# Performance work log

Hardware: AMD Instinct MI355X
Metric: run time of the kernel (lower is better)

The kernel has to match this reference:

```python
import jax, jax.numpy as jnp
import numpy as np
from jax import lax

LATENT = 128
CODEBOOK = 1024

def _conv(x, w, b):
    # NCHW conv, kernel OIHW, stride 1, padding 1 (same)
    y = lax.conv_general_dilated(x, w, (1, 1), ((1, 1), (1, 1)),
                                 dimension_numbers=('NCHW', 'OIHW', 'NCHW'))
    return y + b[None, :, None, None]

def _conv_transpose(x, w, b):
    # ConvTranspose2d(k=3, s=1, p=1) == conv with flipped kernel, in/out swapped, pad 1
    w_eff = jnp.flip(w, (2, 3)).transpose(1, 0, 2, 3)  # [Cin,Cout,3,3] -> [Cout,Cin,3,3]
    return _conv(x, w_eff, b)

def _maxpool2(x):
    return lax.reduce_window(x, -jnp.inf, lax.max, (1, 1, 2, 2), (1, 1, 2, 2), 'VALID')

def _upsample2(x):
    # F.interpolate(scale_factor=2), default nearest
    return jnp.repeat(jnp.repeat(x, 2, axis=2), 2, axis=3)

def setup_inputs() -> dict:
    key = jax.random.key(0)
    ks = jax.random.split(key, 20)
    f = jnp.float32
    inp = {
        'x': jax.random.uniform(ks[0], (8192, 1, 24, 24), dtype=f),
        'conv1_w': jax.random.normal(ks[1], (32, 1, 3, 3), f) * 0.1,
        'conv1_b': jnp.zeros((32,), f),
        'conv2_w': jax.random.normal(ks[2], (64, 32, 3, 3), f) * 0.05,
        'conv2_b': jnp.zeros((64,), f),
        'conv3_w': jax.random.normal(ks[3], (128, 64, 3, 3), f) * 0.04,
        'conv3_b': jnp.zeros((128,), f),
        'enc_fc_w': jax.random.normal(ks[4], (LATENT, 3 * 3 * 128), f) * 0.03,
        'enc_fc_b': jnp.zeros((LATENT,), f),
        'codebook': jax.random.normal(ks[5], (CODEBOOK, LATENT), f),
        'dec_fc_w': jax.random.normal(ks[6], (3 * 3 * 128, LATENT), f) * 0.09,
        'dec_fc_b': jnp.zeros((3 * 3 * 128,), f),
        'dct1_w': jax.random.normal(ks[7], (128, 64, 3, 3), f) * 0.03,  # [Cin,Cout,kh,kw]
        'dct1_b': jnp.zeros((64,), f),
        'dct2_w': jax.random.normal(ks[8], (64, 32, 3, 3), f) * 0.04,
        'dct2_b': jnp.zeros((32,), f),
        'dct3_w': jax.random.normal(ks[9], (32, 1, 3, 3), f) * 0.06,
        'dct3_b': jnp.zeros((1,), f),
    }
    return inp

def reference(x, conv1_w, conv1_b, conv2_w, conv2_b, conv3_w, conv3_b,
              enc_fc_w, enc_fc_b, codebook, dec_fc_w, dec_fc_b,
              dct1_w, dct1_b, dct2_w, dct2_b, dct3_w, dct3_b):
    # ---- Encoder ----
    h = _maxpool2(jax.nn.relu(_conv(x, conv1_w, conv1_b)))     # [B,32,12,12]
    h = _maxpool2(jax.nn.relu(_conv(h, conv2_w, conv2_b)))     # [B,64,6,6]
    h = _maxpool2(jax.nn.relu(_conv(h, conv3_w, conv3_b)))     # [B,128,3,3]
    z = h.reshape(-1, 3 * 3 * 128) @ enc_fc_w.T + enc_fc_b     # [B,128]
    # ---- Quantize (L2 nearest-codeword; matmul-trick distances, same argmin) ----
    d2 = (jnp.sum(z * z, axis=1, keepdims=True)
          - 2.0 * z @ codebook.T
          + jnp.sum(codebook * codebook, axis=1)[None, :])     # [B,K]
    idx = jnp.argmin(d2, axis=1)                               # [B]
    z_q = codebook[idx]                                        # [B,128]
    # ---- Decoder ----
    d = z_q @ dec_fc_w.T + dec_fc_b                            # [B,1152]
    d = d.reshape(-1, 128, 3, 3)
    d = _upsample2(jax.nn.relu(_conv_transpose(d, dct1_w, dct1_b)))  # [B,64,6,6]
    d = _upsample2(jax.nn.relu(_conv_transpose(d, dct2_w, dct2_b)))  # [B,32,12,12]
    d = _upsample2(jax.nn.relu(_conv_transpose(d, dct3_w, dct3_b)))  # [B,1,24,24]
    return d
```

## Files before the change

### kernel.cpp

```cpp
#include <hip/hip_runtime.h>

typedef __attribute__((ext_vector_type(8))) short short8;
typedef __attribute__((ext_vector_type(4))) float f32x4;
typedef unsigned short ushort_t;
typedef unsigned int uint_t;

#define OFF_W1R   0
#define OFF_W2R   288
#define OFF_W3R   (288+18432)
#define OFF_EWT   (18720+73728)
#define OFF_CT    (92448+147456)
#define OFF_CC    (239904+131072)
#define OFF_DWT   (370976+1024)
#define OFF_D1R   (372000+147456)
#define OFF_D2R   (519456+73728)
#define OFF_D3R   (593184+18432)
#define WS_WEIGHTS (611616+288)
#define OFF_W2BF  WS_WEIGHTS
#define OFF_W3BF  (OFF_W2BF+18432)
#define OFF_H     (OFF_W3BF+73728)
#define OFF_TABLE OFF_H
#define OFF_IDSN  (OFF_H+8192*1152)

__device__ __forceinline__ ushort_t f2bf(float v) {
  uint_t u = __float_as_uint(v);
  return (ushort_t)((u + 0x7FFFu + ((u >> 16) & 1u)) >> 16);
}
__device__ __forceinline__ float bf2f(ushort_t b) {
  return __uint_as_float(((uint_t)b) << 16);
}

__global__ void vq_prep(const float* __restrict__ conv1_w, const float* __restrict__ codebook,
                        const float* __restrict__ dec_fc_w,
                        const float* __restrict__ dct1_w, const float* __restrict__ dct2_w,
                        const float* __restrict__ dct3_w, float* __restrict__ ws) {
  int i = blockIdx.x * blockDim.x + threadIdx.x;
  if (i >= WS_WEIGHTS) return;
  if (i < OFF_W2R) {
    int tap = i >> 5, co = i & 31;
    ws[i] = conv1_w[co*9 + tap];
  } else if (i < OFF_CC) {
    return;
  } else if (i < OFF_DWT) {
    int k = i - OFF_CC;
    float s = 0.f;
    for (int j = 0; j < 128; ++j) { float v = codebook[k*128+j]; s += v*v; }
    ws[i] = s;
  } else if (i < OFF_D1R) {
    int l = i - OFF_DWT;
    int j = l % 1152, k = l / 1152;
    ws[i] = dec_fc_w[j*128 + k];
  } else if (i < OFF_D2R) {
    int l = i - OFF_D1R;
    int co = l & 63, r = l >> 6, tap = r % 9, ci = r / 9;
    ws[i] = dct1_w[(ci*64 + co)*9 + (8 - tap)];
  } else if (i < OFF_D3R) {
    int l = i - OFF_D2R;
    int co = l & 31, r = l >> 5, tap = r % 9, ci = r / 9;
    ws[i] = dct2_w[(ci*32 + co)*9 + (8 - tap)];
  } else {
    int l = i - OFF_D3R;
    int tap = l % 9, ci = l / 9;
    ws[i] = dct3_w[ci*9 + (8 - tap)];
  }
}

#define P2_N (92160 + 294912 + 262144)
__global__ void vq_prep2(const float* __restrict__ conv2_w, const float* __restrict__ conv3_w,
                         const float* __restrict__ enc_fc_w, const float* __restrict__ codebook,
                         float* __restrict__ ws) {
  int i = blockIdx.x * blockDim.x + threadIdx.x;
  if (i >= P2_N) return;
  ushort_t* W2 = (ushort_t*)(ws + OFF_W2BF);
  ushort_t* W3 = (ushort_t*)(ws + OFF_W3BF);
  ushort_t* EW = (ushort_t*)(ws + OFF_EWT);
  ushort_t* CB = (ushort_t*)(ws + OFF_CT);
  if (i < 18432) {
    int tap = i >> 11, r = i & 2047, co = r >> 5, ch = r & 31;
    float v = conv2_w[(co*32 + ch)*9 + tap];
    ushort_t hb = f2bf(v);
    W2[i] = hb; W2[18432 + i] = f2bf(v - bf2f(hb));
  } else if (i < 92160) {
    int j = i - 18432;
    int tap = j >> 13, r = j & 8191, co = r >> 6, ch = r & 63;
    float v = conv3_w[(co*64 + ch)*9 + tap];
    ushort_t hb = f2bf(v);
    W3[j] = hb; W3[73728 + j] = f2bf(v - bf2f(hb));
  } else if (i < 92160 + 294912) {
    int e = i - 92160;
    int p = e / 147456, r = e % 147456;
    int kk = r & 31, n = (r >> 5) & 127, ks = r >> 12;
    float v = enc_fc_w[n*1152 + ks*32 + kk];
    ushort_t hb = f2bf(v);
    EW[r] = (p == 0) ? EW[r] : EW[r];
    if (p == 0) EW[r] = hb; else EW[147456 + r] = f2bf(v - bf2f(hb));
  } else {
    int e = i - 92160 - 294912;
    int p = e / 131072, r = e % 131072;
    int kk = r & 31, cw = (r >> 5) & 1023, ks = r >> 15;
    float v = codebook[cw*128 + ks*32 + kk];
    ushort_t hb = f2bf(v);
    if (p == 0) CB[r] = hb; else CB[131072 + r] = f2bf(v - bf2f(hb));
  }
}

__global__ __launch_bounds__(256, 3) void vq_enc(
    const float* __restrict__ x,
    const float* __restrict__ b1, const float* __restrict__ b2, const float* __restrict__ b3,
    const float* __restrict__ ws, ushort_t* __restrict__ hhi, ushort_t* __restrict__ hlo)
{
  __shared__ ushort_t R0h[7840], R0l[7840];
  __shared__ ushort_t C3h[4608], C3l[4608];
  __shared__ float XT[624];
  const int t = threadIdx.x;
  const int b = blockIdx.x;

  for (int i = t; i < 3920; i += 256) { ((uint_t*)R0h)[i] = 0u; ((uint_t*)R0l)[i] = 0u; }
  for (int i = t; i < 2304; i += 256) { ((uint_t*)C3h)[i] = 0u; ((uint_t*)C3l)[i] = 0u; }
  const float* xb = x + (size_t)b * 576;
  for (int i = t; i < 624; i += 256) {
    int row = i / 26, col = i - row * 26;
    XT[i] = (col >= 1 && col <= 24) ? xb[row*24 + col - 1] : 0.f;
  }
  __syncthreads();

  {
    int co = t & 31, g = t >> 5, gy = g >> 1, gx = g & 1;
    float w[9];
    #pragma unroll
    for (int k = 0; k < 9; ++k) w[k] = ws[OFF_W1R + k*32 + co];
    float bias = b1[co];
    #pragma unroll
    for (int pr = 0; pr < 3; ++pr) {
      int Y = gy*6 + pr*2;
      float a0[12], a1[12];
      #pragma unroll
      for (int i = 0; i < 12; ++i) { a0[i] = 0.f; a1[i] = 0.f; }
      #pragma unroll
      for (int wy = 0; wy < 4; ++wy) {
        int ry = Y - 1 + wy;
        if (ry < 0 || ry > 23) continue;
        const float2* rp = (const float2*)&XT[ry*26 + gx*12];
        float r[14];
        #pragma unroll
        for (int k = 0; k < 7; ++k) { float2 p = rp[k]; r[2*k] = p.x; r[2*k+1] = p.y; }
        if (wy < 3) {
          #pragma unroll
          for (int xx = 0; xx < 12; ++xx)
            #pragma unroll
            for (int dx = 0; dx < 3; ++dx) a0[xx] += r[xx+dx] * w[wy*3+dx];
        }
        if (wy >= 1) {
          #pragma unroll
          for (int xx = 0; xx < 12; ++xx)
            #pragma unroll
            for (int dx = 0; dx < 3; ++dx) a1[xx] += r[xx+dx] * w[(wy-1)*3+dx];
        }
      }
      #pragma unroll
      for (int pc = 0; pc < 6; ++pc) {
        float m = fmaxf(fmaxf(a0[2*pc], a0[2*pc+1]), fmaxf(a1[2*pc], a1[2*pc+1]));
        float v = m + bias; v = v > 0.f ? v : 0.f;
        int row = gy*3 + pr, colp = gx*6 + pc;
        int addr = ((row+1)*14 + (colp+1))*40 + co;
        ushort_t hb = f2bf(v);
        R0h[addr] = hb;
        R0l[addr] = f2bf(v - bf2f(hb));
      }
    }
  }
  __syncthreads();

  const int lane = t & 63, quad = lane >> 4, col = lane & 15;
  const int wv = t >> 6;

  {
    const int h = wv & 1, p = wv >> 1;
    const ushort_t* W2 = (const ushort_t*)(ws + OFF_W2BF);
    int baseA[5];
    #pragma unroll
    for (int mi = 0; mi < 5; ++mi) {
      int m = (h*5 + mi)*16 + col; if (m > 143) m = 143;
      int cell = m >> 2, sub = m & 3;
      int opy = cell / 6, opx = cell - opy*6;
      int y = 2*opy + (sub >> 1), xx = 2*opx + (sub & 1);
      baseA[mi] = (y*14 + xx)*40 + quad*8;
    }
    f32x4 acc[5][2];
    #pragma unroll
    for (int mi = 0; mi < 5; ++mi) { acc[mi][0] = (f32x4)0.f; acc[mi][1] = (f32x4)0.f; }
    const int co0 = p*32 + col, co1 = co0 + 16;
    #pragma unroll
    for (int t9 = 0; t9 < 9; ++t9) {
      const int TAPOFF = ((t9/3)*14 + (t9%3))*40;
      int bidx = t9*2048 + quad*8;
      short8 Bh0 = *(const short8*)(W2 + bidx + co0*32);
      short8 Bh1 = *(const short8*)(W2 + bidx + co1*32);
      short8 Bl0 = *(const short8*)(W2 + 18432 + bidx + co0*32);
      short8 Bl1 = *(const short8*)(W2 + 18432 + bidx + co1*32);
      #pragma unroll
      for (int mi = 0; mi < 5; ++mi) {
        int a = baseA[mi] + TAPOFF;
        short8 Ah = *(const short8*)(R0h + a);
        short8 Al = *(const short8*)(R0l + a);
        acc[mi][0] = __builtin_amdgcn_mfma_f32_16x16x32_bf16(Al, Bh0, acc[mi][0], 0, 0, 0);
        acc[mi][0] = __builtin_amdgcn_mfma_f32_16x16x32_bf16(Ah, Bl0, acc[mi][0], 0, 0, 0);
        acc[mi][0] = __builtin_amdgcn_mfma_f32_16x16x32_bf16(Ah, Bh0, acc[mi][0], 0, 0, 0);
        acc[mi][1] = __builtin_amdgcn_mfma_f32_16x16x32_bf16(Al, Bh1, acc[mi][1], 0, 0, 0);
        acc[mi][1] = __builtin_amdgcn_mfma_f32_16x16x32_bf16(Ah, Bl1, acc[mi][1], 0, 0, 0);
        acc[mi][1] = __builtin_amdgcn_mfma_f32_16x16x32_bf16(Ah, Bh1, acc[mi][1], 0, 0, 0);
      }
    }
    #pragma unroll
    for (int mi = 0; mi < 5; ++mi) {
      int cell = (h*5 + mi)*4 + quad;
      if (cell < 36) {
        int opy = cell / 6, opx = cell - opy*6;
        int wa = ((opy+1)*8 + (opx+1))*72;
        #pragma unroll
        for (int j = 0; j < 2; ++j) {
          int ch = j ? co1 : co0;
          f32x4 a = acc[mi][j];
          float v = fmaxf(fmaxf(a.x, a.y), fmaxf(a.z, a.w)) + b2[ch];
          v = v > 0.f ? v : 0.f;
          ushort_t hb = f2bf(v);
          C3h[wa + ch] = hb;
          C3l[wa + ch] = f2bf(v - bf2f(hb));
        }
      }
    }
  }
  __syncthreads();

  {
    const ushort_t* W3 = (const ushort_t*)(ws + OFF_W3BF);
    int baseA[3];
    #pragma unroll
    for (int mt = 0; mt < 3; ++mt) {
      int m = mt*16 + col; if (m > 35) m = 35;
      int cell = m >> 2, sub = m & 3;
      int opy = cell / 3, opx = cell - opy*3;
      int y = 2*opy + (sub >> 1), xx = 2*opx + (sub & 1);
      baseA[mt] = (y*8 + xx)*72 + quad*8;
    }
    f32x4 acc[3][2];
    #pragma unroll
    for (int mt = 0; mt < 3; ++mt) { acc[mt][0] = (f32x4)0.f; acc[mt][1] = (f32x4)0.f; }
    const int co0 = wv*16 + col, co1 = co0 + 64;
    #pragma unroll
    for (int ks = 0; ks < 18; ++ks) {
      const int t9 = ks >> 1, ch0 = (ks & 1)*32;
      const int TAPOFF = ((t9/3)*8 + (t9%3))*72;
      int bidx = t9*8192 + ch0 + quad*8;
      short8 Bh0 = *(const short8*)(W3 + bidx + co0*64);
      short8 Bh1 = *(const short8*)(W3 + bidx + co1*64);
      short8 Bl0 = *(const short8*)(W3 + 73728 + bidx + co0*64);
      short8 Bl1 = *(const short8*)(W3 + 73728 + bidx + co1*64);
      #pragma unroll
      for (int mt = 0; mt < 3; ++mt) {
        int a = baseA[mt] + TAPOFF + ch0;
        short8 Ah = *(const short8*)(C3h + a);
        short8 Al = *(const short8*)(C3l + a);
        acc[mt][0] = __builtin_amdgcn_mfma_f32_16x16x32_bf16(Al, Bh0, acc[mt][0], 0, 0, 0);
        acc[mt][0] = __builtin_amdgcn_mfma_f32_16x16x32_bf16(Ah, Bl0, acc[mt][0], 0, 0, 0);
        acc[mt][0] = __builtin_amdgcn_mfma_f32_16x16x32_bf16(Ah, Bh0, acc[mt][0], 0, 0, 0);
        acc[mt][1] = __builtin_amdgcn_mfma_f32_16x16x32_bf16(Al, Bh1, acc[mt][1], 0, 0, 0);
        acc[mt][1] = __builtin_amdgcn_mfma_f32_16x16x32_bf16(Ah, Bl1, acc[mt][1], 0, 0, 0);
        acc[mt][1] = __builtin_amdgcn_mfma_f32_16x16x32_bf16(Ah, Bh1, acc[mt][1], 0, 0, 0);
      }
    }
    ushort_t* hb_ = hhi + (size_t)b * 1152;
    ushort_t* lb_ = hlo + (size_t)b * 1152;
    #pragma unroll
    for (int mt = 0; mt < 3; ++mt) {
      int cell = mt*4 + quad;
      if (cell < 9) {
        #pragma unroll
        for (int j = 0; j < 2; ++j) {
          int ch = j ? co1 : co0;
          f32x4 a = acc[mt][j];
          float v = fmaxf(fmaxf(a.x, a.y), fmaxf(a.z, a.w)) + b3[ch];
          v = v > 0.f ? v : 0.f;
          ushort_t hb2 = f2bf(v);
          hb_[ch*9 + cell] = hb2;
          lb_[ch*9 + cell] = f2bf(v - bf2f(hb2));
        }
      }
    }
  }
}

__global__ __launch_bounds__(256, 4) void vq_fc_argmin(
    const float* __restrict__ efb, const float* __restrict__ ws,
    const ushort_t* __restrict__ hhi, const ushort_t* __restrict__ hlo,
    int* __restrict__ ids)
{
  __shared__ float ZL[16*132];
  __shared__ float WVs[64];
  __shared__ int   WIs[64];
  const int t = threadIdx.x;
  const int sb = blockIdx.x * 16;
  const int lane = t & 63, wv = t >> 6;
  const int col = lane & 15, quad = lane >> 4;

  const ushort_t* EW  = (const ushort_t*)(ws + OFF_EWT);
  const ushort_t* CBB = (const ushort_t*)(ws + OFF_CT);

  f32x4 acc0 = (f32x4)0.f, acc1 = (f32x4)0.f;
  const size_t hrow = (size_t)(sb + col) * 1152 + quad*8;
  #pragma unroll 4
  for (int ks = 0; ks < 36; ++ks) {
    short8 Ah = *(const short8*)(hhi + hrow + ks*32);
    short8 Al = *(const short8*)(hlo + hrow + ks*32);
    int n0 = wv*32 + col, n1 = n0 + 16;
    const ushort_t* bp0 = EW + (ks*128 + n0)*32 + quad*8;
    const ushort_t* bp1 = EW + (ks*128 + n1)*32 + quad*8;
    short8 Bh0 = *(const short8*)(bp0);
    short8 Bl0 = *(const short8*)(bp0 + 147456);
    short8 Bh1 = *(const short8*)(bp1);
    short8 Bl1 = *(const short8*)(bp1 + 147456);
    acc0 = __builtin_amdgcn_mfma_f32_16x16x32_bf16(Al, Bh0, acc0, 0, 0, 0);
    acc0 = __builtin_amdgcn_mfma_f32_16x16x32_bf16(Ah, Bl0, acc0, 0, 0, 0);
    acc0 = __builtin_amdgcn_mfma_f32_16x16x32_bf16(Ah, Bh0, acc0, 0, 0, 0);
    acc1 = __builtin_amdgcn_mfma_f32_16x16x32_bf16(Al, Bh1, acc1, 0, 0, 0);
    acc1 = __builtin_amdgcn_mfma_f32_16x16x32_bf16(Ah, Bl1, acc1, 0, 0, 0);
    acc1 = __builtin_amdgcn_mfma_f32_16x16x32_bf16(Ah, Bh1, acc1, 0, 0, 0);
  }
  {
    int n0 = wv*32 + col, n1 = n0 + 16;
    float bs0 = efb[n0], bs1 = efb[n1];
    #pragma unroll
    for (int r = 0; r < 4; ++r) {
      int m = quad*4 + r;
      ZL[m*132 + n0] = acc0[r] + bs0;
      ZL[m*132 + n1] = acc1[r] + bs1;
    }
  }
  __syncthreads();

  short8 zAh[4], zAl[4];
  #pragma unroll
  for (int ks = 0; ks < 4; ++ks) {
    const float* zp = &ZL[col*132 + ks*32 + quad*8];
    float4 z0 = *(const float4*)zp;
    float4 z1 = *(const float4*)(zp + 4);
    float zv[8] = {z0.x, z0.y, z0.z, z0.w, z1.x, z1.y, z1.z, z1.w};
    ushort_t ph[8], pl[8];
    #pragma unroll
    for (int e = 0; e < 8; ++e) {
      ushort_t hb = f2bf(zv[e]);
      ph[e] = hb; pl[e] = f2bf(zv[e] - bf2f(hb));
    }
    zAh[ks] = *(const short8*)ph;
    zAl[ks] = *(const short8*)pl;
  }

  float bestv[4]; int besti[4];
  #pragma unroll
  for (int r = 0; r < 4; ++r) { bestv[r] = 3.4e38f; besti[r] = 0; }
  for (int c4 = 0; c4 < 4; ++c4) {
    f32x4 dacc[4];
    #pragma unroll
    for (int nn = 0; nn < 4; ++nn) dacc[nn] = (f32x4)0.f;
    #pragma unroll
    for (int ks = 0; ks < 4; ++ks) {
      #pragma unroll
      for (int nn = 0; nn < 4; ++nn) {
        int cw = (wv*16 + c4*4 + nn)*16 + col;
        const ushort_t* bp = CBB + (size_t)(ks*1024 + cw)*32 + quad*8;
        short8 Bh = *(const short8*)bp;
        short8 Bl = *(const short8*)(bp + 131072);
        dacc[nn] = __builtin_amdgcn_mfma_f32_16x16x32_bf16(zAl[ks], Bh, dacc[nn], 0, 0, 0);
        dacc[nn] = __builtin_amdgcn_mfma_f32_16x16x32_bf16(zAh[ks], Bl, dacc[nn], 0, 0, 0);
        dacc[nn] = __builtin_amdgcn_mfma_f32_16x16x32_bf16(zAh[ks], Bh, dacc[nn], 0, 0, 0);
      }
    }
    #pragma unroll
    for (int nn = 0; nn < 4; ++nn) {
      int cw = (wv*16 + c4*4 + nn)*16 + col;
      float ccv = ws[OFF_CC + cw];
      #pragma unroll
      for (int r = 0; r < 4; ++r) {
        float dist = ccv - 2.f*dacc[nn][r];
        if (dist < bestv[r]) { bestv[r] = dist; besti[r] = cw; }
      }
    }
  }

  #pragma unroll
  for (int r = 0; r < 4; ++r) {
    float v = bestv[r]; int ii = besti[r];
    #pragma unroll
    for (int off = 8; off >= 1; off >>= 1) {
      float v2 = __shfl_xor(v, off); int i2 = __shfl_xor(ii, off);
      if (v2 < v || (v2 == v && i2 < ii)) { v = v2; ii = i2; }
    }
    if (col == 0) {
      int m = quad*4 + r;
      WVs[wv*16 + m] = v; WIs[wv*16 + m] = ii;
    }
  }
  __syncthreads();
  if (t < 16) {
    float v = WVs[t]; int ii = WIs[t];
    #pragma unroll
    for (int w2 = 1; w2 < 4; ++w2) {
      float v2 = WVs[w2*16 + t]; int i2 = WIs[w2*16 + t];
      if (v2 < v || (v2 == v && i2 < ii)) { v = v2; ii = i2; }
    }
    ids[sb + t] = ii;
  }
}

__global__ __launch_bounds__(256, 4) void vq_dec_table(
    const float* __restrict__ codebook, const float* __restrict__ decb,
    const float* __restrict__ d1b, const float* __restrict__ d2b, const float* __restrict__ d3b,
    const float* __restrict__ ws, float* __restrict__ table)
{
  __shared__ float DB[1152];
  __shared__ float R1[2432];
  __shared__ float R0[4736];
  __shared__ float ZQ[128];
  const int t = threadIdx.x;
  const int cw = blockIdx.x;

  if (t < 128) ZQ[t] = codebook[(size_t)cw*128 + t];
  __syncthreads();

  #pragma unroll
  for (int p = 0; p < 5; ++p) {
    int j = t + p*256;
    if (j < 1152) {
      float a0 = decb[j];
      const float* wb = ws + OFF_DWT + j;
      #pragma unroll 4
      for (int k = 0; k < 128; ++k) a0 += wb[k*1152] * ZQ[k];
      DB[j] = a0;
    }
  }
  __syncthreads();

  {
    int co = t & 63, g = t >> 6;
    float a9[9];
    #pragma unroll
    for (int i = 0; i < 9; ++i) a9[i] = 0.f;
    const float* wbase = ws + OFF_D1R + co;
    for (int ci = g*32; ci < g*32+32; ++ci) {
      float w[9];
      #pragma unroll
      for (int k = 0; k < 9; ++k) w[k] = wbase[(ci*9+k)*64];
      const float* fin = DB + ci*9;
      #pragma unroll
      for (int ry = 0; ry < 3; ++ry) {
        float r[5];
        r[0] = 0.f; r[4] = 0.f;
        r[1] = fin[ry*3]; r[2] = fin[ry*3+1]; r[3] = fin[ry*3+2];
        #pragma unroll
        for (int y = 0; y < 3; ++y) {
          int d = ry - y + 1;
          if (d >= 0 && d < 3) {
            #pragma unroll
            for (int xx = 0; xx < 3; ++xx)
              #pragma unroll
              for (int dx = 0; dx < 3; ++dx) a9[y*3+xx] += r[xx+dx] * w[d*3+dx];
          }
        }
      }
    }
    __syncthreads();
    if (g) {
      #pragma unroll
      for (int i = 0; i < 9; ++i) R0[((g-1)*64 + co)*9 + i] = a9[i];
    }
    __syncthreads();
    if (!g) {
      float bias = d1b[co];
      #pragma unroll
      for (int i = 0; i < 9; ++i)
        a9[i] += R0[co*9 + i] + R0[(64+co)*9 + i] + R0[(128+co)*9 + i];
      #pragma unroll
      for (int yy = 0; yy < 3; ++yy)
        #pragma unroll
        for (int xx = 0; xx < 3; ++xx) {
          float v = a9[yy*3+xx] + bias; v = v > 0.f ? v : 0.f;
          int base = co*38 + (2*yy)*6 + 2*xx;
          R1[base] = v; R1[base+1] = v; R1[base+6] = v; R1[base+7] = v;
        }
    }
  }
  __syncthreads();

  {
    int co = t & 31, hh = (t >> 5) & 1, g = t >> 6;
    int sy = g >> 1, sx = g & 1;
    float a9[9];
    #pragma unroll
    for (int i = 0; i < 9; ++i) a9[i] = 0.f;
    const float* wbase = ws + OFF_D2R + co;
    for (int ci = hh*32; ci < hh*32+32; ++ci) {
      float w[9];
      #pragma unroll
      for (int k = 0; k < 9; ++k) w[k] = wbase[(ci*9+k)*32];
      const float* base = &R1[ci*38];
      #pragma unroll
      for (int wy = 0; wy < 5; ++wy) {
        int ry = sy*3 - 1 + wy;
        if (ry < 0 || ry > 5) continue;
        const float* row = base + ry*6 + sx*3;
        float r[5];
        if (sx == 0) {
          r[0] = 0.f; r[1] = row[0]; r[2] = row[1]; r[3] = row[2]; r[4] = row[3];
        } else {
          r[0] = row[-1]; r[1] = row[0]; r[2] = row[1]; r[3] = row[2]; r[4] = 0.f;
        }
        #pragma unroll
        for (int y = 0; y < 3; ++y) {
          int d = wy - 1 - y + 1;
          if (d >= 0 && d < 3) {
            #pragma unroll
            for (int xx = 0; xx < 3; ++xx)
              #pragma unroll
              for (int dx = 0; dx < 3; ++dx) a9[y*3+xx] += r[xx+dx] * w[d*3+dx];
          }
        }
      }
    }
    __syncthreads();
    if (hh) {
      #pragma unroll
      for (int i = 0; i < 9; ++i) DB[(g*32 + co)*9 + i] = a9[i];
    }
    __syncthreads();
    if (!hh) {
      float bias = d2b[co];
      #pragma unroll
      for (int i = 0; i < 9; ++i) a9[i] += DB[(g*32 + co)*9 + i];
      #pragma unroll
      for (int yy = 0; yy < 3; ++yy)
        #pragma unroll
        for (int xx = 0; xx < 3; ++xx) {
          float v = a9[yy*3+xx] + bias; v = v > 0.f ? v : 0.f;
          int rr = sy*3 + yy, cc_ = sx*3 + xx;
          int base = co*146 + (2*rr)*12 + 2*cc_;
          R0[base] = v; R0[base+1] = v; R0[base+12] = v; R0[base+13] = v;
        }
    }
  }
  __syncthreads();

  if (t < 144) {
    int yy = t / 12, xx = t - yy*12;
    const float* w3 = ws + OFF_D3R;
    float acc = d3b[0];
    for (int ci = 0; ci < 32; ++ci) {
      const float* base = &R0[ci*146];
      #pragma unroll
      for (int dy = 0; dy < 3; ++dy) {
        int ry = yy - 1 + dy;
        int ryc = ry < 0 ? 0 : (ry > 11 ? 11 : ry);
        bool rok = (ry >= 0 && ry < 12);
        #pragma unroll
        for (int dx = 0; dx < 3; ++dx) {
          int rx = xx - 1 + dx;
          int rxc = rx < 0 ? 0 : (rx > 11 ? 11 : rx);
          float v = base[ryc*12 + rxc];
          v = (rok && rx >= 0 && rx < 12) ? v : 0.f;
          acc += v * w3[ci*9 + dy*3 + dx];
        }
      }
    }
    float v = acc > 0.f ? acc : 0.f;
    float* ob = table + (size_t)cw * 576;
    int o0 = (2*yy)*24 + 2*xx;
    ob[o0] = v; ob[o0+1] = v; ob[o0+24] = v; ob[o0+25] = v;
  }
}

__global__ __launch_bounds__(256, 8) void vq_scatter(
    const float* __restrict__ table, const int* __restrict__ ids,
    float* __restrict__ out, int nvec)
{
  int idx = blockIdx.x * 256 + threadIdx.x;
  if (idx >= nvec) return;
  int b = idx / 144;
  int r = idx - b * 144;
  int cw = ids[b];
  ((float4*)out)[idx] = ((const float4*)(table + (size_t)cw * 576))[r];
}

extern "C" void kernel_launch(void* const* d_in, const int* in_sizes, int n_in,
                              void* d_out, int out_size, void* d_ws, size_t ws_size,
                              hipStream_t stream) {
  const float* x   = (const float*)d_in[0];
  const float* c1w = (const float*)d_in[1];
  const float* c1b = (const float*)d_in[2];
  const float* c2w = (const float*)d_in[3];
  const float* c2b = (const float*)d_in[4];
  const float* c3w = (const float*)d_in[5];
  const float* c3b = (const float*)d_in[6];
  const float* efw = (const float*)d_in[7];
  const float* efb = (const float*)d_in[8];
  const float* cb  = (const float*)d_in[9];
  const float* dfw = (const float*)d_in[10];
  const float* dfb = (const float*)d_in[11];
  const float* dw1 = (const float*)d_in[12];
  const float* db1 = (const float*)d_in[13];
  const float* dw2 = (const float*)d_in[14];
  const float* db2 = (const float*)d_in[15];
  const float* dw3 = (const float*)d_in[16];
  const float* db3 = (const float*)d_in[17];
  float* ws = (float*)d_ws;
  ushort_t* hhi  = (ushort_t*)(ws + OFF_H);
  ushort_t* hlo  = hhi + (size_t)8192*1152;
  float* table = ws + OFF_TABLE;
  int*   ids   = (int*)(ws + OFF_IDSN);
  float* outp = (float*)d_out;
  int B = in_sizes[0] / 576;

  vq_prep<<<(WS_WEIGHTS + 255) / 256, 256, 0, stream>>>(c1w, cb, dfw, dw1, dw2, dw3, ws);
  vq_prep2<<<(P2_N + 255) / 256, 256, 0, stream>>>(c2w, c3w, efw, cb, ws);
  vq_enc<<<B, 256, 0, stream>>>(x, c1b, c2b, c3b, ws, hhi, hlo);
  vq_fc_argmin<<<B/16, 256, 0, stream>>>(efb, ws, hhi, hlo, ids);
  vq_dec_table<<<1024, 256, 0, stream>>>(cb, dfb, db1, db2, db3, ws, table);
  int nvec = B * 144;
  vq_scatter<<<(nvec + 255) / 256, 256, 0, stream>>>(table, ids, outp, nvec);
}
```

Measured before the change: 634.1 us.

## Move decoder table convs to split-bf16 MFMA and re-layout encoder LDS tiles

The per-codeword decoder table kernel now runs the first two transposed convolutions as implicit GEMMs on MFMA, using three bf16 hi/lo products per step, with weights pre-split by the prep kernel. The scalar FP32 loops are dropped and the last conv reads an upsampled, padded channel-last buffer. The encoder's shared-memory activations are reorganised into channel-group-major tiles that hold 8 channels per pixel, and conv1 writes packed channel pairs, which shrinks LDS use and may cut bank conflicts. The split-bf16 scheme gives slightly different rounding than FP32.

```diff
diff --git a/kernel.cpp b/kernel.cpp
--- a/kernel.cpp
+++ b/kernel.cpp
@@ -6,8 +6,8 @@
 typedef unsigned int uint_t;
 
 #define OFF_W1R   0
-#define OFF_W2R   288
-#define OFF_W3R   (288+18432)
+#define OFF_BD2F  288
+#define OFF_BD1F  18720
 #define OFF_EWT   (18720+73728)
 #define OFF_CT    (92448+147456)
 #define OFF_CC    (239904+131072)
@@ -31,12 +31,11 @@
 }
 
 __global__ void vq_prep(const float* __restrict__ conv1_w, const float* __restrict__ codebook,
-                        const float* __restrict__ dec_fc_w,
-                        const float* __restrict__ dct1_w, const float* __restrict__ dct2_w,
-                        const float* __restrict__ dct3_w, float* __restrict__ ws) {
+                        const float* __restrict__ dec_fc_w, const float* __restrict__ dct3_w,
+                        float* __restrict__ ws) {
   int i = blockIdx.x * blockDim.x + threadIdx.x;
   if (i >= WS_WEIGHTS) return;
-  if (i < OFF_W2R) {
+  if (i < OFF_BD2F) {
     int tap = i >> 5, co = i & 31;
     ws[i] = conv1_w[co*9 + tap];
   } else if (i < OFF_CC) {
@@ -50,31 +49,28 @@
     int l = i - OFF_DWT;
     int j = l % 1152, k = l / 1152;
     ws[i] = dec_fc_w[j*128 + k];
-  } else if (i < OFF_D2R) {
-    int l = i - OFF_D1R;
-    int co = l & 63, r = l >> 6, tap = r % 9, ci = r / 9;
-    ws[i] = dct1_w[(ci*64 + co)*9 + (8 - tap)];
   } else if (i < OFF_D3R) {
-    int l = i - OFF_D2R;
-    int co = l & 31, r = l >> 5, tap = r % 9, ci = r / 9;
-    ws[i] = dct2_w[(ci*32 + co)*9 + (8 - tap)];
-  } else {
+    return;
+  } else if (i < WS_WEIGHTS) {
     int l = i - OFF_D3R;
     int tap = l % 9, ci = l / 9;
     ws[i] = dct3_w[ci*9 + (8 - tap)];
   }
 }
 
-#define P2_N (92160 + 294912 + 262144)
+#define P2_N (92160 + 294912 + 262144 + 73728 + 18432)
 __global__ void vq_prep2(const float* __restrict__ conv2_w, const float* __restrict__ conv3_w,
                          const float* __restrict__ enc_fc_w, const float* __restrict__ codebook,
+                         const float* __restrict__ dct1_w, const float* __restrict__ dct2_w,
                          float* __restrict__ ws) {
   int i = blockIdx.x * blockDim.x + threadIdx.x;
   if (i >= P2_N) return;
-  ushort_t* W2 = (ushort_t*)(ws + OFF_W2BF);
-  ushort_t* W3 = (ushort_t*)(ws + OFF_W3BF);
-  ushort_t* EW = (ushort_t*)(ws + OFF_EWT);
-  ushort_t* CB = (ushort_t*)(ws + OFF_CT);
+  ushort_t* W2  = (ushort_t*)(ws + OFF_W2BF);
+  ushort_t* W3  = (ushort_t*)(ws + OFF_W3BF);
+  ushort_t* EW  = (ushort_t*)(ws + OFF_EWT);
+  ushort_t* CB  = (ushort_t*)(ws + OFF_CT);
+  ushort_t* BD1 = (ushort_t*)(ws + OFF_BD1F);
+  ushort_t* BD2 = (ushort_t*)(ws + OFF_BD2F);
   if (i < 18432) {
     int tap = i >> 11, r = i & 2047, co = r >> 5, ch = r & 31;
     float v = conv2_w[(co*32 + ch)*9 + tap];
@@ -86,21 +82,34 @@
     float v = conv3_w[(co*64 + ch)*9 + tap];
     ushort_t hb = f2bf(v);
     W3[j] = hb; W3[73728 + j] = f2bf(v - bf2f(hb));
-  } else if (i < 92160 + 294912) {
-    int e = i - 92160;
-    int p = e / 147456, r = e % 147456;
+  } else if (i < 387072) {
+    int r = i - 92160;
+    int p = r / 147456; r %= 147456;
     int kk = r & 31, n = (r >> 5) & 127, ks = r >> 12;
     float v = enc_fc_w[n*1152 + ks*32 + kk];
     ushort_t hb = f2bf(v);
-    EW[r] = (p == 0) ? EW[r] : EW[r];
     if (p == 0) EW[r] = hb; else EW[147456 + r] = f2bf(v - bf2f(hb));
-  } else {
-    int e = i - 92160 - 294912;
-    int p = e / 131072, r = e % 131072;
+  } else if (i < 649216) {
+    int r = i - 387072;
+    int p = r / 131072; r %= 131072;
     int kk = r & 31, cw = (r >> 5) & 1023, ks = r >> 15;
     float v = codebook[cw*128 + ks*32 + kk];
     ushort_t hb = f2bf(v);
     if (p == 0) CB[r] = hb; else CB[131072 + r] = f2bf(v - bf2f(hb));
+  } else if (i < 722944) {
+    int r = i - 649216;
+    int co = r / 1152, k = r - co*1152;
+    int tap = k >> 7, ci = k & 127;
+    float v = dct1_w[(ci*64 + co)*9 + (8 - tap)];
+    ushort_t hb = f2bf(v);
+    BD1[r] = hb; BD1[73728 + r] = f2bf(v - bf2f(hb));
+  } else {
+    int r = i - 722944;
+    int co = r / 576, k = r - co*576;
+    int tap = k >> 6, ci = k & 63;
+    float v = dct2_w[(ci*32 + co)*9 + (8 - tap)];
+    ushort_t hb = f2bf(v);
+    BD2[r] = hb; BD2[18432 + r] = f2bf(v - bf2f(hb));
   }
 }
 
@@ -109,63 +118,81 @@
     const float* __restrict__ b1, const float* __restrict__ b2, const float* __restrict__ b3,
     const float* __restrict__ ws, ushort_t* __restrict__ hhi, ushort_t* __restrict__ hlo)
 {
-  __shared__ ushort_t R0h[7840], R0l[7840];
-  __shared__ ushort_t C3h[4608], C3l[4608];
+  __shared__ ushort_t R0h[6272], R0l[6272];
+  __shared__ ushort_t A2h[5120], A2l[5120];
   __shared__ float XT[624];
   const int t = threadIdx.x;
   const int b = blockIdx.x;
 
-  for (int i = t; i < 3920; i += 256) { ((uint_t*)R0h)[i] = 0u; ((uint_t*)R0l)[i] = 0u; }
-  for (int i = t; i < 2304; i += 256) { ((uint_t*)C3h)[i] = 0u; ((uint_t*)C3l)[i] = 0u; }
+  for (int i = t; i < 3136; i += 256) { ((uint_t*)R0h)[i] = 0u; ((uint_t*)R0l)[i] = 0u; }
+  for (int i = t; i < 2560; i += 256) { ((uint_t*)A2h)[i] = 0u; ((uint_t*)A2l)[i] = 0u; }
   const float* xb = x + (size_t)b * 576;
   for (int i = t; i < 624; i += 256) {
-    int row = i / 26, col = i - row * 26;
-    XT[i] = (col >= 1 && col <= 24) ? xb[row*24 + col - 1] : 0.f;
+    int row = i / 26, c = i - row * 26;
+    XT[i] = (c >= 1 && c <= 24) ? xb[row*24 + c - 1] : 0.f;
   }
   __syncthreads();
 
   {
-    int co = t & 31, g = t >> 5, gy = g >> 1, gx = g & 1;
-    float w[9];
-    #pragma unroll
-    for (int k = 0; k < 9; ++k) w[k] = ws[OFF_W1R + k*32 + co];
-    float bias = b1[co];
+    int cp = t & 15, g = t >> 4;
+    int gy = g >> 2, gx = g & 3;
+    float wgt[2][9], bs[2];
+    #pragma unroll
+    for (int c = 0; c < 2; ++c) {
+      bs[c] = b1[2*cp + c];
+      #pragma unroll
+      for (int k = 0; k < 9; ++k) wgt[c][k] = ws[OFF_W1R + k*32 + 2*cp + c];
+    }
+    int quadc = cp >> 2, coff = (cp & 3) * 2;
     #pragma unroll
     for (int pr = 0; pr < 3; ++pr) {
-      int Y = gy*6 + pr*2;
-      float a0[12], a1[12];
-      #pragma unroll
-      for (int i = 0; i < 12; ++i) { a0[i] = 0.f; a1[i] = 0.f; }
+      int Y = (gy*3 + pr)*2;
+      float a0[2][6], a1[2][6];
+      #pragma unroll
+      for (int c = 0; c < 2; ++c)
+        #pragma unroll
+        for (int i = 0; i < 6; ++i) { a0[c][i] = 0.f; a1[c][i] = 0.f; }
       #pragma unroll
       for (int wy = 0; wy < 4; ++wy) {
         int ry = Y - 1 + wy;
         if (ry < 0 || ry > 23) continue;
-        const float2* rp = (const float2*)&XT[ry*26 + gx*12];
-        float r[14];
+        const float2* rp = (const float2*)&XT[ry*26 + gx*6];
+        float r[8];
         #pragma unroll
-        for (int k = 0; k < 7; ++k) { float2 p = rp[k]; r[2*k] = p.x; r[2*k+1] = p.y; }
+        for (int k = 0; k < 4; ++k) { float2 p = rp[k]; r[2*k] = p.x; r[2*k+1] = p.y; }
         if (wy < 3) {
           #pragma unroll
-          for (int xx = 0; xx < 12; ++xx)
+          for (int c = 0; c < 2; ++c)
             #pragma unroll
-            for (int dx = 0; dx < 3; ++dx) a0[xx] += r[xx+dx] * w[wy*3+dx];
+            for (int xx = 0; xx < 6; ++xx)
+              #pragma unroll
+              for (int dx = 0; dx < 3; ++dx) a0[c][xx] += r[xx+dx] * wgt[c][wy*3+dx];
         }
         if (wy >= 1) {
           #pragma unroll
-          for (int xx = 0; xx < 12; ++xx)
+          for (int c = 0; c < 2; ++c)
             #pragma unroll
-            for (int dx = 0; dx < 3; ++dx) a1[xx] += r[xx+dx] * w[(wy-1)*3+dx];
+            for (int xx = 0; xx < 6; ++xx)
+              #pragma unroll
+              for (int dx = 0; dx < 3; ++dx) a1[c][xx] += r[xx+dx] * wgt[c][(wy-1)*3+dx];
         }
       }
       #pragma unroll
-      for (int pc = 0; pc < 6; ++pc) {
-        float m = fmaxf(fmaxf(a0[2*pc], a0[2*pc+1]), fmaxf(a1[2*pc], a1[2*pc+1]));
-        float v = m + bias; v = v > 0.f ? v : 0.f;
-        int row = gy*3 + pr, colp = gx*6 + pc;
-        int addr = ((row+1)*14 + (colp+1))*40 + co;
-        ushort_t hb = f2bf(v);
-        R0h[addr] = hb;
-        R0l[addr] = f2bf(v - bf2f(hb));
+      for (int pc = 0; pc < 3; ++pc) {
+        uint_t hi = 0, lo = 0;
+        #pragma unroll
+        for (int c = 0; c < 2; ++c) {
+          float m = fmaxf(fmaxf(a0[c][2*pc], a0[c][2*pc+1]), fmaxf(a1[c][2*pc], a1[c][2*pc+1]));
+          float v = m + bs[c]; v = v > 0.f ? v : 0.f;
+          ushort_t hb = f2bf(v);
+          ushort_t lb = f2bf(v - bf2f(hb));
+          hi |= ((uint_t)hb) << (16*c);
+          lo |= ((uint_t)lb) << (16*c);
+        }
+        int p = (gy*3 + pr + 1)*14 + (gx*3 + pc + 1);
+        int base = quadc*1568 + p*8 + coff;
+        ((uint_t*)R0h)[base >> 1] = hi;
+        ((uint_t*)R0l)[base >> 1] = lo;
       }
     }
   }
@@ -177,14 +204,14 @@
   {
     const int h = wv & 1, p = wv >> 1;
     const ushort_t* W2 = (const ushort_t*)(ws + OFF_W2BF);
-    int baseA[5];
+    int pA[5];
     #pragma unroll
     for (int mi = 0; mi < 5; ++mi) {
       int m = (h*5 + mi)*16 + col; if (m > 143) m = 143;
       int cell = m >> 2, sub = m & 3;
       int opy = cell / 6, opx = cell - opy*6;
       int y = 2*opy + (sub >> 1), xx = 2*opx + (sub & 1);
-      baseA[mi] = (y*14 + xx)*40 + quad*8;
+      pA[mi] = y*14 + xx;
     }
     f32x4 acc[5][2];
     #pragma unroll
@@ -192,7 +219,7 @@
     const int co0 = p*32 + col, co1 = co0 + 16;
     #pragma unroll
     for (int t9 = 0; t9 < 9; ++t9) {
-      const int TAPOFF = ((t9/3)*14 + (t9%3))*40;
+      const int toff = (t9/3)*14 + (t9%3);
       int bidx = t9*2048 + quad*8;
       short8 Bh0 = *(const short8*)(W2 + bidx + co0*32);
       short8 Bh1 = *(const short8*)(W2 + bidx + co1*32);
@@ -200,7 +227,7 @@
       short8 Bl1 = *(const short8*)(W2 + 18432 + bidx + co1*32);
       #pragma unroll
       for (int mi = 0; mi < 5; ++mi) {
-        int a = baseA[mi] + TAPOFF;
+        int a = quad*1568 + (pA[mi] + toff)*8;
         short8 Ah = *(const short8*)(R0h + a);
         short8 Al = *(const short8*)(R0l + a);
         acc[mi][0] = __builtin_amdgcn_mfma_f32_16x16x32_bf16(Al, Bh0, acc[mi][0], 0, 0, 0);
@@ -216,7 +243,7 @@
       int cell = (h*5 + mi)*4 + quad;
       if (cell < 36) {
         int opy = cell / 6, opx = cell - opy*6;
-        int wa = ((opy+1)*8 + (opx+1))*72;
+        int p2 = (opy+1)*10 + (opx+1);
         #pragma unroll
         for (int j = 0; j < 2; ++j) {
           int ch = j ? co1 : co0;
@@ -224,8 +251,9 @@
           float v = fmaxf(fmaxf(a.x, a.y), fmaxf(a.z, a.w)) + b2[ch];
           v = v > 0.f ? v : 0.f;
           ushort_t hb = f2bf(v);
-          C3h[wa + ch] = hb;
-          C3l[wa + ch] = f2bf(v - bf2f(hb));
+          int wa = (ch >> 3)*640 + p2*8 + (ch & 7);
+          A2h[wa] = hb;
+          A2l[wa] = f2bf(v - bf2f(hb));
         }
       }
     }
@@ -234,14 +262,14 @@
 
   {
     const ushort_t* W3 = (const ushort_t*)(ws + OFF_W3BF);
-    int baseA[3];
+    int pA[3];
     #pragma unroll
     for (int mt = 0; mt < 3; ++mt) {
       int m = mt*16 + col; if (m > 35) m = 35;
       int cell = m >> 2, sub = m & 3;
       int opy = cell / 3, opx = cell - opy*3;
       int y = 2*opy + (sub >> 1), xx = 2*opx + (sub & 1);
-      baseA[mt] = (y*8 + xx)*72 + quad*8;
+      pA[mt] = y*10 + xx;
     }
     f32x4 acc[3][2];
     #pragma unroll
@@ -249,8 +277,9 @@
     const int co0 = wv*16 + col, co1 = co0 + 64;
     #pragma unroll
     for (int ks = 0; ks < 18; ++ks) {
-      const int t9 = ks >> 1, ch0 = (ks & 1)*32;
-      const int TAPOFF = ((t9/3)*8 + (t9%3))*72;
+      const int t9 = ks >> 1, half = ks & 1, ch0 = half*32;
+      const int toff = (t9/3)*10 + (t9%3);
+      const int grp = half*4 + quad;
       int bidx = t9*8192 + ch0 + quad*8;
       short8 Bh0 = *(const short8*)(W3 + bidx + co0*64);
       short8 Bh1 = *(const short8*)(W3 + bidx + co1*64);
@@ -258,9 +287,9 @@
       short8 Bl1 = *(const short8*)(W3 + 73728 + bidx + co1*64);
       #pragma unroll
       for (int mt = 0; mt < 3; ++mt) {
-        int a = baseA[mt] + TAPOFF + ch0;
-        short8 Ah = *(const short8*)(C3h + a);
-        short8 Al = *(const short8*)(C3l + a);
+        int a = grp*640 + (pA[mt] + toff)*8;
+        short8 Ah = *(const short8*)(A2h + a);
+        short8 Al = *(const short8*)(A2l + a);
         acc[mt][0] = __builtin_amdgcn_mfma_f32_16x16x32_bf16(Al, Bh0, acc[mt][0], 0, 0, 0);
         acc[mt][0] = __builtin_amdgcn_mfma_f32_16x16x32_bf16(Ah, Bl0, acc[mt][0], 0, 0, 0);
         acc[mt][0] = __builtin_amdgcn_mfma_f32_16x16x32_bf16(Ah, Bh0, acc[mt][0], 0, 0, 0);
@@ -417,13 +446,21 @@
     const float* __restrict__ d1b, const float* __restrict__ d2b, const float* __restrict__ d3b,
     const float* __restrict__ ws, float* __restrict__ table)
 {
-  __shared__ float DB[1152];
-  __shared__ float R1[2432];
-  __shared__ float R0[4736];
+  __shared__ float POOL[8008];
+  __shared__ float PS[1536];
   __shared__ float ZQ[128];
+  ushort_t* FAh = (ushort_t*)POOL;
+  ushort_t* FAl = FAh + 3400;
+  ushort_t* GAh = (ushort_t*)(POOL + 3400);
+  ushort_t* GAl = GAh + 4608;
+  float* R2 = POOL;
+
   const int t = threadIdx.x;
   const int cw = blockIdx.x;
-
+  const int lane = t & 63, wv = t >> 6;
+  const int col = lane & 15, quad = lane >> 4;
+
+  for (int i = t; i < 8008; i += 256) POOL[i] = 0.f;
   if (t < 128) ZQ[t] = codebook[(size_t)cw*128 + t];
   __syncthreads();
 
@@ -435,116 +472,112 @@
       const float* wb = ws + OFF_DWT + j;
       #pragma unroll 4
       for (int k = 0; k < 128; ++k) a0 += wb[k*1152] * ZQ[k];
-      DB[j] = a0;
-    }
-  }
-  __syncthreads();
-
+      int ci = j / 9, rem = j - ci*9;
+      int pix = ((rem/3)+1)*5 + (rem%3) + 1;
+      ushort_t hb = f2bf(a0);
+      FAh[pix*136 + ci] = hb;
+      FAl[pix*136 + ci] = f2bf(a0 - bf2f(hb));
+    }
+  }
+  __syncthreads();
+
+  const ushort_t* BD1 = (const ushort_t*)(ws + OFF_BD1F);
+  f32x4 acc1 = (f32x4)0.f;
   {
-    int co = t & 63, g = t >> 6;
-    float a9[9];
-    #pragma unroll
-    for (int i = 0; i < 9; ++i) a9[i] = 0.f;
-    const float* wbase = ws + OFF_D1R + co;
-    for (int ci = g*32; ci < g*32+32; ++ci) {
-      float w[9];
-      #pragma unroll
-      for (int k = 0; k < 9; ++k) w[k] = wbase[(ci*9+k)*64];
-      const float* fin = DB + ci*9;
-      #pragma unroll
-      for (int ry = 0; ry < 3; ++ry) {
-        float r[5];
-        r[0] = 0.f; r[4] = 0.f;
-        r[1] = fin[ry*3]; r[2] = fin[ry*3+1]; r[3] = fin[ry*3+2];
-        #pragma unroll
-        for (int y = 0; y < 3; ++y) {
-          int d = ry - y + 1;
-          if (d >= 0 && d < 3) {
-            #pragma unroll
-            for (int xx = 0; xx < 3; ++xx)
-              #pragma unroll
-              for (int dx = 0; dx < 3; ++dx) a9[y*3+xx] += r[xx+dx] * w[d*3+dx];
-          }
+    const int m9 = col < 9 ? col : 8;
+    const int oy = m9/3, ox = m9 - oy*3;
+    const int co = wv*16 + col;
+    #pragma unroll 4
+    for (int ks = 0; ks < 36; ++ks) {
+      int kb = ks*32 + quad*8;
+      int tap = kb >> 7, ci0 = kb & 127;
+      int pix = (oy + tap/3)*5 + ox + tap%3;
+      short8 Ah = *(const short8*)(FAh + pix*136 + ci0);
+      short8 Al = *(const short8*)(FAl + pix*136 + ci0);
+      const ushort_t* bp = BD1 + co*1152 + kb;
+      short8 Bh = *(const short8*)bp;
+      short8 Bl = *(const short8*)(bp + 73728);
+      acc1 = __builtin_amdgcn_mfma_f32_16x16x32_bf16(Al, Bh, acc1, 0, 0, 0);
+      acc1 = __builtin_amdgcn_mfma_f32_16x16x32_bf16(Ah, Bl, acc1, 0, 0, 0);
+      acc1 = __builtin_amdgcn_mfma_f32_16x16x32_bf16(Ah, Bh, acc1, 0, 0, 0);
+    }
+  }
+  {
+    const int co = wv*16 + col;
+    float bias = d1b[co];
+    #pragma unroll
+    for (int r = 0; r < 4; ++r) {
+      int m = quad*4 + r;
+      if (m < 9) {
+        int oy = m/3, ox = m - oy*3;
+        float v = acc1[r] + bias; v = v > 0.f ? v : 0.f;
+        ushort_t hb = f2bf(v), lb = f2bf(v - bf2f(hb));
+        int rbase = (2*oy+1)*8 + (2*ox+1);
+        GAh[(rbase  )*72 + co] = hb; GAh[(rbase+1)*72 + co] = hb;
+        GAh[(rbase+8)*72 + co] = hb; GAh[(rbase+9)*72 + co] = hb;
+        GAl[(rbase  )*72 + co] = lb; GAl[(rbase+1)*72 + co] = lb;
+        GAl[(rbase+8)*72 + co] = lb; GAl[(rbase+9)*72 + co] = lb;
+      }
+    }
+  }
+  __syncthreads();
+
+  const ushort_t* BD2 = (const ushort_t*)(ws + OFF_BD2F);
+  f32x4 acc2[3];
+  acc2[0] = (f32x4)0.f; acc2[1] = (f32x4)0.f; acc2[2] = (f32x4)0.f;
+  const int h = wv >> 1, js = (wv & 1)*3;
+  for (int ks = h*9; ks < h*9 + 9; ++ks) {
+    int kb = ks*32 + quad*8;
+    int tap = kb >> 6, ci0 = kb & 63;
+    int ty = tap/3, tx = tap - ty*3;
+    #pragma unroll
+    for (int jj = 0; jj < 3; ++jj) {
+      int job = js + jj;
+      int mt = job >> 1, nt = job & 1;
+      int m = mt*16 + col; if (m > 35) m = 35;
+      int oy = m/6, ox = m - oy*6;
+      int pix = (oy+ty)*8 + ox+tx;
+      short8 Ah = *(const short8*)(GAh + pix*72 + ci0);
+      short8 Al = *(const short8*)(GAl + pix*72 + ci0);
+      int co = nt*16 + col;
+      const ushort_t* bp = BD2 + co*576 + kb;
+      short8 Bh = *(const short8*)bp;
+      short8 Bl = *(const short8*)(bp + 18432);
+      acc2[jj] = __builtin_amdgcn_mfma_f32_16x16x32_bf16(Al, Bh, acc2[jj], 0, 0, 0);
+      acc2[jj] = __builtin_amdgcn_mfma_f32_16x16x32_bf16(Ah, Bl, acc2[jj], 0, 0, 0);
+      acc2[jj] = __builtin_amdgcn_mfma_f32_16x16x32_bf16(Ah, Bh, acc2[jj], 0, 0, 0);
+    }
+  }
+  __syncthreads();
+  if (h == 1) {
+    #pragma unroll
+    for (int jj = 0; jj < 3; ++jj) {
+      int job = js + jj;
+      #pragma unroll
+      for (int r = 0; r < 4; ++r) PS[(job*64 + lane)*4 + r] = acc2[jj][r];
+    }
+  }
+  for (int i = t; i < 6468; i += 256) R2[i] = 0.f;
+  __syncthreads();
+  if (h == 0) {
+    #pragma unroll
+    for (int jj = 0; jj < 3; ++jj) {
+      int job = js + jj;
+      int mt = job >> 1, nt = job & 1;
+      int co = nt*16 + col;
+      float bias = d2b[co];
+      #pragma unroll
+      for (int r = 0; r < 4; ++r) {
+        float v = acc2[jj][r] + PS[(job*64 + lane)*4 + r];
+        int m = mt*16 + quad*4 + r;
+        if (m < 36) {
+          int oy = m/6, ox = m - oy*6;
+          v += bias; v = v > 0.f ? v : 0.f;
+          int rbase = (2*oy+1)*14 + (2*ox+1);
+          R2[(rbase   )*33 + co] = v; R2[(rbase+ 1)*33 + co] = v;
+          R2[(rbase+14)*33 + co] = v; R2[(rbase+15)*33 + co] = v;
         }
       }
-    }
-    __syncthreads();
-    if (g) {
-      #pragma unroll
-      for (int i = 0; i < 9; ++i) R0[((g-1)*64 + co)*9 + i] = a9[i];
-    }
-    __syncthreads();
-    if (!g) {
-      float bias = d1b[co];
-      #pragma unroll
-      for (int i = 0; i < 9; ++i)
-        a9[i] += R0[co*9 + i] + R0[(64+co)*9 + i] + R0[(128+co)*9 + i];
-      #pragma unroll
-      for (int yy = 0; yy < 3; ++yy)
-        #pragma unroll
-        for (int xx = 0; xx < 3; ++xx) {
-          float v = a9[yy*3+xx] + bias; v = v > 0.f ? v : 0.f;
-          int base = co*38 + (2*yy)*6 + 2*xx;
-          R1[base] = v; R1[base+1] = v; R1[base+6] = v; R1[base+7] = v;
-        }
-    }
-  }
-  __syncthreads();
-
-  {
-    int co = t & 31, hh = (t >> 5) & 1, g = t >> 6;
-    int sy = g >> 1, sx = g & 1;
-    float a9[9];
-    #pragma unroll
-    for (int i = 0; i < 9; ++i) a9[i] = 0.f;
-    const float* wbase = ws + OFF_D2R + co;
-    for (int ci = hh*32; ci < hh*32+32; ++ci) {
-      float w[9];
-      #pragma unroll
-      for (int k = 0; k < 9; ++k) w[k] = wbase[(ci*9+k)*32];
-      const float* base = &R1[ci*38];
-      #pragma unroll
-      for (int wy = 0; wy < 5; ++wy) {
-        int ry = sy*3 - 1 + wy;
-        if (ry < 0 || ry > 5) continue;
-        const float* row = base + ry*6 + sx*3;
-        float r[5];
-        if (sx == 0) {
-          r[0] = 0.f; r[1] = row[0]; r[2] = row[1]; r[3] = row[2]; r[4] = row[3];
-        } else {
-          r[0] = row[-1]; r[1] = row[0]; r[2] = row[1]; r[3] = row[2]; r[4] = 0.f;
-        }
-        #pragma unroll
-        for (int y = 0; y < 3; ++y) {
-          int d = wy - 1 - y + 1;
-          if (d >= 0 && d < 3) {
-            #pragma unroll
-            for (int xx = 0; xx < 3; ++xx)
-              #pragma unroll
-              for (int dx = 0; dx < 3; ++dx) a9[y*3+xx] += r[xx+dx] * w[d*3+dx];
-          }
-        }
-      }
-    }
-    __syncthreads();
-    if (hh) {
-      #pragma unroll
-      for (int i = 0; i < 9; ++i) DB[(g*32 + co)*9 + i] = a9[i];
-    }
-    __syncthreads();
-    if (!hh) {
-      float bias = d2b[co];
-      #pragma unroll
-      for (int i = 0; i < 9; ++i) a9[i] += DB[(g*32 + co)*9 + i];
-      #pragma unroll
-      for (int yy = 0; yy < 3; ++yy)
-        #pragma unroll
-        for (int xx = 0; xx < 3; ++xx) {
-          float v = a9[yy*3+xx] + bias; v = v > 0.f ? v : 0.f;
-          int rr = sy*3 + yy, cc_ = sx*3 + xx;
-          int base = co*146 + (2*rr)*12 + 2*cc_;
-          R0[base] = v; R0[base+1] = v; R0[base+12] = v; R0[base+13] = v;
-        }
     }
   }
   __syncthreads();
@@ -553,23 +586,15 @@
     int yy = t / 12, xx = t - yy*12;
     const float* w3 = ws + OFF_D3R;
     float acc = d3b[0];
-    for (int ci = 0; ci < 32; ++ci) {
-      const float* base = &R0[ci*146];
-      #pragma unroll
-      for (int dy = 0; dy < 3; ++dy) {
-        int ry = yy - 1 + dy;
-        int ryc = ry < 0 ? 0 : (ry > 11 ? 11 : ry);
-        bool rok = (ry >= 0 && ry < 12);
-        #pragma unroll
-        for (int dx = 0; dx < 3; ++dx) {
-          int rx = xx - 1 + dx;
-          int rxc = rx < 0 ? 0 : (rx > 11 ? 11 : rx);
-          float v = base[ryc*12 + rxc];
-          v = (rok && rx >= 0 && rx < 12) ? v : 0.f;
-          acc += v * w3[ci*9 + dy*3 + dx];
-        }
-      }
-    }
+    #pragma unroll
+    for (int dy = 0; dy < 3; ++dy)
+      #pragma unroll
+      for (int dx = 0; dx < 3; ++dx) {
+        const float* rp = &R2[((yy+dy)*14 + xx+dx)*33];
+        const float* wp = w3 + dy*3 + dx;
+        #pragma unroll 8
+        for (int ci = 0; ci < 32; ++ci) acc += rp[ci] * wp[ci*9];
+      }
     float v = acc > 0.f ? acc : 0.f;
     float* ob = table + (size_t)cw * 576;
     int o0 = (2*yy)*24 + 2*xx;
@@ -618,8 +643,8 @@
   float* outp = (float*)d_out;
   int B = in_sizes[0] / 576;
 
-  vq_prep<<<(WS_WEIGHTS + 255) / 256, 256, 0, stream>>>(c1w, cb, dfw, dw1, dw2, dw3, ws);
-  vq_prep2<<<(P2_N + 255) / 256, 256, 0, stream>>>(c2w, c3w, efw, cb, ws);
+  vq_prep<<<(WS_WEIGHTS + 255) / 256, 256, 0, stream>>>(c1w, cb, dfw, dw3, ws);
+  vq_prep2<<<(P2_N + 255) / 256, 256, 0, stream>>>(c2w, c3w, efw, cb, dw1, dw2, ws);
   vq_enc<<<B, 256, 0, stream>>>(x, c1b, c2b, c3b, ws, hhi, hlo);
   vq_fc_argmin<<<B/16, 256, 0, stream>>>(efb, ws, hhi, hlo, ids);
   vq_dec_table<<<1024, 256, 0, stream>>>(cb, dfb, db1, db2, db3, ws, table);
```

Result: no change. 633.2 us (-0.1%).
